# Kernel optimization log

Hardware: AMD Instinct MI355X
Metric: run time of the kernel (lower is better)

## Reference

```python
import jax, jax.numpy as jnp
import numpy as np

# Dims: B=batch, N_IN=input capsules, D_IN=input capsule dim,
#       J=output capsules (nb_capsules), C=output capsule dim (capsule_size)
B, N_IN, D_IN, J, C = 32, 2048, 16, 64, 32
ITERS = 5
EPS = 1e-7  # K.epsilon()


def squash(v):
    # Keras code: vector += eps; norm = sum(v^2, -1, keepdims); v * norm/(1+norm)/sqrt(norm)
    v = v + EPS
    n = jnp.sum(v * v, axis=-1, keepdims=True)
    return v * (n / (1.0 + n) / jnp.sqrt(n))


def setup_inputs() -> dict:
    key = jax.random.key(0)
    k1, k2 = jax.random.split(key)
    x = jax.random.normal(k1, (B, N_IN, D_IN, 1), dtype=jnp.float32)
    # glorot_uniform over fan_in=D_IN (last axis), fan_out=C
    limit = float(np.sqrt(6.0 / (D_IN + C)))
    W = jax.random.uniform(k2, (N_IN, J, C, D_IN), dtype=jnp.float32,
                           minval=-limit, maxval=limit)
    return {"x": x, "W": W}


def reference(x, W):
    # x: (B, N_IN, D_IN, 1) -> u: (B, N_IN, D_IN)
    u = x[..., 0]
    # Prediction vectors u_hat[b,i,j] = W[i,j] @ u[b,i] : (B, N_IN, J, C)
    u_hat = jnp.einsum('bid,ijcd->bijc', u, W)
    # Routing logits b_ij: (B, N_IN, J)
    b = jnp.zeros(u_hat.shape[:3], dtype=u_hat.dtype)
    v = None
    for i in range(ITERS):
        c = jax.nn.softmax(b, axis=1)              # softmax over input capsules (axis=1 in source)
        s = jnp.einsum('bij,bijc->bjc', c, u_hat)   # weighted sum over i -> (B, J, C)
        v = squash(s)                                # squash over capsule vector dim C
        if i < ITERS - 1:
            # agreement update: b += <v_j, u_hat_ij>
            b = b + jnp.einsum('bjc,bijc->bij', v, u_hat)
    # match compute_output_shape (B, nb_capsules, capsule_size, 1)
    return v[..., None]
```

## Files before the change

### kernel.cpp

```cpp
#include <hip/hip_runtime.h>
#include <hip/hip_bf16.h>

#define B_ 32
#define N_ 2048
#define D_ 16
#define J_ 64
#define C_ 32
#define NCHUNK 32
#define ICHUNK 64
#define IPW    16

typedef __attribute__((ext_vector_type(8)))  short short8;
typedef __attribute__((ext_vector_type(4)))  short s16x4;
typedef __attribute__((ext_vector_type(16))) float f32x16;
typedef __attribute__((ext_vector_type(4)))  float f32x4;
typedef __attribute__((ext_vector_type(16))) int   i32x16;
typedef __attribute__((ext_vector_type(2)))  long  longx2;

using bf16_t = __hip_bfloat16;

__global__ __launch_bounds__(256) void prep_u_kernel(const float* __restrict__ x,
                                                     bf16_t* __restrict__ ut,
                                                     signed char* __restrict__ uq,
                                                     float* __restrict__ su) {
  int t = blockIdx.x * 256 + threadIdx.x;
  int b = t & 31;
  int i = t >> 5;
  const float* xp = x + (size_t)(b * N_ + i) * D_;
  float v[16];
  *(f32x4*)(v)      = *(const f32x4*)(xp);
  *(f32x4*)(v + 4)  = *(const f32x4*)(xp + 4);
  *(f32x4*)(v + 8)  = *(const f32x4*)(xp + 8);
  *(f32x4*)(v + 12) = *(const f32x4*)(xp + 12);

  float m = 0.f;
#pragma unroll
  for (int k = 0; k < 16; ++k) m = fmaxf(m, fabsf(v[k]));
  m = fmaxf(m, 1e-20f);
  float inv = 127.0f / m;
  union { longx2 l2; signed char c[16]; } pk;
#pragma unroll
  for (int k = 0; k < 16; ++k) pk.c[k] = (signed char)__float2int_rn(v[k] * inv);
  *(longx2*)(uq + (size_t)t * D_) = pk.l2;
  su[t] = m * (1.0f / 127.0f);

  union { short8 s; bf16_t h[8]; } o0, o1;
#pragma unroll
  for (int k = 0; k < 8; ++k) { o0.h[k] = __float2bfloat16(v[k]); o1.h[k] = __float2bfloat16(v[8 + k]); }
  *(short8*)(ut + (size_t)t * D_)     = o0.s;
  *(short8*)(ut + (size_t)t * D_ + 8) = o1.s;
}

template<int MODE>
__global__ __launch_bounds__(256) void pass_kernel(
    const float*        __restrict__ Wf,
    const signed char*  __restrict__ Wq,
    signed char*        __restrict__ Wqo,
    float*              __restrict__ SWo,
    const float*        __restrict__ SW,
    const signed char*  __restrict__ uq,
    const float*        __restrict__ su,
    const bf16_t*       __restrict__ ut,
    const float*        __restrict__ V,
    float*              __restrict__ PS,
    float*              __restrict__ PZ)
{
  constexpr bool UNIFORM = (MODE == 0 || MODE == 2);
  constexpr bool INT8    = (MODE == 0 || MODE == 1);

  const int tid  = threadIdx.x;
  const int w    = tid >> 6;
  const int lane = tid & 63;
  const int half = lane >> 5;
  const int lc   = lane & 31;

  const int j  = blockIdx.x / NCHUNK;
  const int ch = blockIdx.x % NCHUNK;

  int crow[16];
#pragma unroll
  for (int r = 0; r < 16; ++r) crow[r] = (r & 3) + 4 * half + 8 * (r >> 2);

  float Vreg[16];
  if (!UNIFORM) {
#pragma unroll
    for (int r = 0; r < 16; ++r) Vreg[r] = V[(lc * J_ + j) * C_ + crow[r]];
  }

  float S[16];
#pragma unroll
  for (int r = 0; r < 16; ++r) S[r] = 0.f;
  float zacc = 0.f;

  const int ibase = ch * ICHUNK + w * IPW;
  const int frag_off = lc * D_ + half * 8;

  if constexpr (INT8) {
    const i32x16 zi = {0,0,0,0,0,0,0,0,0,0,0,0,0,0,0,0};
    for (int t = 0; t < IPW; ++t) {
      const int i = ibase + t;
      long ul = *(const long*)(uq + (size_t)i * (B_ * D_) + frag_off);
      const size_t tile = ((size_t)i * J_ + j) * (C_ * D_);
      long wl;
      float sw_i;
      if constexpr (MODE == 0) {
        const float* wp = Wf + tile + frag_off;
        f32x4 w0 = *(const f32x4*)(wp);
        f32x4 w1 = *(const f32x4*)(wp + 4);
        float wv[8] = {w0.x, w0.y, w0.z, w0.w, w1.x, w1.y, w1.z, w1.w};
        float m = 0.f;
#pragma unroll
        for (int k = 0; k < 8; ++k) m = fmaxf(m, fabsf(wv[k]));
        m = fmaxf(m, __shfl_xor(m, 1));
        m = fmaxf(m, __shfl_xor(m, 2));
        m = fmaxf(m, __shfl_xor(m, 4));
        m = fmaxf(m, __shfl_xor(m, 8));
        m = fmaxf(m, __shfl_xor(m, 16));
        m = fmaxf(m, __shfl_xor(m, 32));
        m = fmaxf(m, 1e-20f);
        float qs = 127.0f / m;
        union { long l; signed char c[8]; } pk;
#pragma unroll
        for (int k = 0; k < 8; ++k) pk.c[k] = (signed char)__float2int_rn(wv[k] * qs);
        wl = pk.l;
        sw_i = m * (1.0f / 127.0f);
        *(long*)(Wqo + tile + frag_off) = wl;
        if (lane == 0) SWo[(size_t)i * J_ + j] = sw_i;
      } else {
        wl = *(const long*)(Wq + tile + frag_off);
        sw_i = SW[(size_t)i * J_ + j];
      }
      const float s = sw_i * su[i * B_ + lc];

      i32x16 iacc = __builtin_amdgcn_mfma_i32_32x32x16_i8(wl, ul, zi, 0, 0, 0);

      if constexpr (UNIFORM) {
#pragma unroll
        for (int r = 0; r < 16; ++r) S[r] = fmaf(s, (float)iacc[r], S[r]);
      } else {
        float af[16];
        float ph = 0.f;
#pragma unroll
        for (int r = 0; r < 16; ++r) { af[r] = (float)iacc[r]; ph = fmaf(Vreg[r], af[r], ph); }
        ph *= s;
        ph += __shfl_xor(ph, 32);
        float e = __expf(ph);
        zacc += e;
        float es = e * s;
#pragma unroll
        for (int r = 0; r < 16; ++r) S[r] = fmaf(es, af[r], S[r]);
      }
    }
  } else {
    const f32x16 zeroacc = {0,0,0,0,0,0,0,0,0,0,0,0,0,0,0,0};
    for (int t = 0; t < IPW; ++t) {
      const int i = ibase + t;
      short8 ufrag = *(const short8*)(ut + (size_t)i * (B_ * D_) + frag_off);
      const size_t tile = ((size_t)i * J_ + j) * (C_ * D_);
      const float* wp = Wf + tile + frag_off;
      f32x4 w0 = *(const f32x4*)(wp);
      f32x4 w1 = *(const f32x4*)(wp + 4);
      union { short8 v; bf16_t h[8]; } cv;
      cv.h[0] = __float2bfloat16(w0.x);
      cv.h[1] = __float2bfloat16(w0.y);
      cv.h[2] = __float2bfloat16(w0.z);
      cv.h[3] = __float2bfloat16(w0.w);
      cv.h[4] = __float2bfloat16(w1.x);
      cv.h[5] = __float2bfloat16(w1.y);
      cv.h[6] = __float2bfloat16(w1.z);
      cv.h[7] = __float2bfloat16(w1.w);
      short8 wfrag = cv.v;

      f32x16 acc = __builtin_amdgcn_mfma_f32_32x32x16_bf16(wfrag, ufrag, zeroacc, 0, 0, 0);

      if constexpr (UNIFORM) {
#pragma unroll
        for (int r = 0; r < 16; ++r) S[r] += acc[r];
      } else {
        float ph = 0.f;
#pragma unroll
        for (int r = 0; r < 16; ++r) ph = fmaf(Vreg[r], acc[r], ph);
        ph += __shfl_xor(ph, 32);
        float e = __expf(ph);
        zacc += e;
#pragma unroll
        for (int r = 0; r < 16; ++r) S[r] = fmaf(e, acc[r], S[r]);
      }
    }
  }

  __shared__ float S_lds[4 * 32 * 33];
  __shared__ float Z_lds[4 * 32];
#pragma unroll
  for (int r = 0; r < 16; ++r)
    S_lds[w * 1056 + lc * 33 + crow[r]] = S[r];
  if (!half)
    Z_lds[w * 32 + lc] = UNIFORM ? (float)IPW : zacc;
  __syncthreads();

  const size_t pbase = (size_t)blockIdx.x * 1024;
  for (int e = tid; e < 1024; e += 256) {
    int b = e >> 5, c = e & 31;
    PS[pbase + e] = S_lds[b * 33 + c] + S_lds[1056 + b * 33 + c] +
                    S_lds[2112 + b * 33 + c] + S_lds[3168 + b * 33 + c];
  }
  if (tid < 32)
    PZ[(size_t)blockIdx.x * 32 + tid] =
        Z_lds[tid] + Z_lds[32 + tid] + Z_lds[64 + tid] + Z_lds[96 + tid];
}

__global__ __launch_bounds__(256) void combine_kernel(
    const float* __restrict__ PS, const float* __restrict__ PZ,
    float* __restrict__ V, float* __restrict__ out, int first, int last)
{
  int t  = blockIdx.x * 256 + threadIdx.x;
  int c  = t & 31;
  int bj = t >> 5;
  int b  = bj >> 6;
  int j  = bj & 63;
  float s = 0.f, zz = 0.f;
#pragma unroll
  for (int ch = 0; ch < NCHUNK; ++ch) {
    s  += PS[(size_t)(j * NCHUNK + ch) * 1024 + b * 32 + c];
    zz += PZ[(j * NCHUNK + ch) * 32 + b];
  }
  float sv = s / zz + 1e-7f;
  float n = sv * sv;
  n += __shfl_xor(n, 1);
  n += __shfl_xor(n, 2);
  n += __shfl_xor(n, 4);
  n += __shfl_xor(n, 8);
  n += __shfl_xor(n, 16);
  float f = n / ((1.f + n) * sqrtf(n));
  float v = sv * f;
  float Vn = first ? v : (V[t] + v);
  V[t] = Vn;
  if (last) out[t] = v;
}

extern "C" void kernel_launch(void* const* d_in, const int* in_sizes, int n_in,
                              void* d_out, int out_size, void* d_ws, size_t ws_size,
                              hipStream_t stream)
{
  const float* x  = (const float*)d_in[0];
  const float* Wf = (const float*)d_in[1];
  float* out = (float*)d_out;
  char* ws = (char*)d_ws;

  const size_t SZ_WQ = (size_t)N_ * J_ * C_ * D_;
  const size_t SZ_SW = (size_t)N_ * J_ * 4;
  const size_t SZ_UQ = (size_t)N_ * B_ * D_;
  const size_t SZ_SU = (size_t)N_ * B_ * 4;
  const size_t SZ_UT = (size_t)N_ * B_ * D_ * 2;
  const size_t SZ_V  = (size_t)B_ * J_ * C_ * 4;
  const size_t SZ_PS = (size_t)J_ * NCHUNK * B_ * C_ * 4;
  const size_t SZ_PZ = (size_t)J_ * NCHUNK * B_ * 4;

  const bool big = ws_size >= SZ_WQ + SZ_SW + SZ_UQ + SZ_SU + SZ_UT + SZ_V + SZ_PS + SZ_PZ;
  char* p = ws;
  signed char* Wq = nullptr;
  float* SWp = nullptr;
  if (big) {
    Wq  = (signed char*)p; p += SZ_WQ;
    SWp = (float*)p;       p += SZ_SW;
  }
  signed char* uq = (signed char*)p; p += SZ_UQ;
  float* su = (float*)p;             p += SZ_SU;
  bf16_t* ut = (bf16_t*)p;           p += SZ_UT;
  float*  V  = (float*)p;            p += SZ_V;
  float*  PS = (float*)p;            p += SZ_PS;
  float*  PZ = (float*)p;

  prep_u_kernel<<<dim3((N_ * B_) / 256), dim3(256), 0, stream>>>(x, ut, uq, su);

  dim3 gA(J_ * NCHUNK), blk(256), gB((B_ * J_ * C_) / 256);
  if (big) {
    pass_kernel<0><<<gA, blk, 0, stream>>>(Wf, nullptr, Wq, SWp, nullptr, uq, su, ut, nullptr, PS, PZ);
    combine_kernel<<<gB, blk, 0, stream>>>(PS, PZ, V, out, 1, 0);
    for (int it = 1; it < 5; ++it) {
      pass_kernel<1><<<gA, blk, 0, stream>>>(nullptr, Wq, nullptr, nullptr, SWp, uq, su, ut, V, PS, PZ);
      combine_kernel<<<gB, blk, 0, stream>>>(PS, PZ, V, out, 0, it == 4 ? 1 : 0);
    }
  } else {
    pass_kernel<2><<<gA, blk, 0, stream>>>(Wf, nullptr, nullptr, nullptr, nullptr, uq, su, ut, nullptr, PS, PZ);
    combine_kernel<<<gB, blk, 0, stream>>>(PS, PZ, V, out, 1, 0);
    for (int it = 1; it < 5; ++it) {
      pass_kernel<3><<<gA, blk, 0, stream>>>(Wf, nullptr, nullptr, nullptr, nullptr, uq, su, ut, V, PS, PZ);
      combine_kernel<<<gB, blk, 0, stream>>>(PS, PZ, V, out, 0, it == 4 ? 1 : 0);
    }
  }
}
```

Baseline: 513.9 us.

## Split W quantization into a separate kernel and prefetch int8 operands in pass loop

Moves the per-call fp32-to-int8 quantization of W out of the first routing pass into a dedicated grid-stride prep kernel, so that pass reads int8 weights like the later passes. The int8 pass loop now software-pipelines its loads, fetching the next weight fragment, u fragment and scale while the current MFMA and accumulation run. The prep kernel adds a launch and makes the first pass re-read the int8 weights it just wrote, in exchange for a simpler, better-overlapped inner loop in all five passes.

```diff
diff --git a/kernel.cpp b/kernel.cpp
--- a/kernel.cpp
+++ b/kernel.cpp
@@ -51,12 +51,40 @@
   *(short8*)(ut + (size_t)t * D_ + 8) = o1.s;
 }
 
+__global__ __launch_bounds__(256) void prep_w_kernel(const float* __restrict__ Wf,
+                                                     signed char* __restrict__ Wq,
+                                                     float* __restrict__ SW) {
+  const int lane = threadIdx.x & 63;
+  const int wid  = (blockIdx.x * 256 + threadIdx.x) >> 6;
+  const int nw   = gridDim.x * 4;
+  for (int tile = wid; tile < N_ * J_; tile += nw) {
+    const float* wp = Wf + (size_t)tile * (C_ * D_) + lane * 8;
+    f32x4 a = *(const f32x4*)wp;
+    f32x4 b = *(const f32x4*)(wp + 4);
+    float wv[8] = {a.x, a.y, a.z, a.w, b.x, b.y, b.z, b.w};
+    float m = 0.f;
+#pragma unroll
+    for (int k = 0; k < 8; ++k) m = fmaxf(m, fabsf(wv[k]));
+    m = fmaxf(m, __shfl_xor(m, 1));
+    m = fmaxf(m, __shfl_xor(m, 2));
+    m = fmaxf(m, __shfl_xor(m, 4));
+    m = fmaxf(m, __shfl_xor(m, 8));
+    m = fmaxf(m, __shfl_xor(m, 16));
+    m = fmaxf(m, __shfl_xor(m, 32));
+    m = fmaxf(m, 1e-20f);
+    float qs = 127.0f / m;
+    union { long l; signed char c[8]; } pk;
+#pragma unroll
+    for (int k = 0; k < 8; ++k) pk.c[k] = (signed char)__float2int_rn(wv[k] * qs);
+    *(long*)(Wq + (size_t)tile * (C_ * D_) + lane * 8) = pk.l;
+    if (lane == 0) SW[tile] = m * (1.0f / 127.0f);
+  }
+}
+
 template<int MODE>
 __global__ __launch_bounds__(256) void pass_kernel(
     const float*        __restrict__ Wf,
     const signed char*  __restrict__ Wq,
-    signed char*        __restrict__ Wqo,
-    float*              __restrict__ SWo,
     const float*        __restrict__ SW,
     const signed char*  __restrict__ uq,
     const float*        __restrict__ su,
@@ -97,59 +125,36 @@
 
   if constexpr (INT8) {
     const i32x16 zi = {0,0,0,0,0,0,0,0,0,0,0,0,0,0,0,0};
+    long wl = *(const long*)(Wq + ((size_t)ibase * J_ + j) * (C_ * D_) + frag_off);
+    long ul = *(const long*)(uq + (size_t)ibase * (B_ * D_) + frag_off);
+    float sc = SW[(size_t)ibase * J_ + j] * su[ibase * B_ + lc];
+
     for (int t = 0; t < IPW; ++t) {
-      const int i = ibase + t;
-      long ul = *(const long*)(uq + (size_t)i * (B_ * D_) + frag_off);
-      const size_t tile = ((size_t)i * J_ + j) * (C_ * D_);
-      long wl;
-      float sw_i;
-      if constexpr (MODE == 0) {
-        const float* wp = Wf + tile + frag_off;
-        f32x4 w0 = *(const f32x4*)(wp);
-        f32x4 w1 = *(const f32x4*)(wp + 4);
-        float wv[8] = {w0.x, w0.y, w0.z, w0.w, w1.x, w1.y, w1.z, w1.w};
-        float m = 0.f;
-#pragma unroll
-        for (int k = 0; k < 8; ++k) m = fmaxf(m, fabsf(wv[k]));
-        m = fmaxf(m, __shfl_xor(m, 1));
-        m = fmaxf(m, __shfl_xor(m, 2));
-        m = fmaxf(m, __shfl_xor(m, 4));
-        m = fmaxf(m, __shfl_xor(m, 8));
-        m = fmaxf(m, __shfl_xor(m, 16));
-        m = fmaxf(m, __shfl_xor(m, 32));
-        m = fmaxf(m, 1e-20f);
-        float qs = 127.0f / m;
-        union { long l; signed char c[8]; } pk;
-#pragma unroll
-        for (int k = 0; k < 8; ++k) pk.c[k] = (signed char)__float2int_rn(wv[k] * qs);
-        wl = pk.l;
-        sw_i = m * (1.0f / 127.0f);
-        *(long*)(Wqo + tile + frag_off) = wl;
-        if (lane == 0) SWo[(size_t)i * J_ + j] = sw_i;
-      } else {
-        wl = *(const long*)(Wq + tile + frag_off);
-        sw_i = SW[(size_t)i * J_ + j];
-      }
-      const float s = sw_i * su[i * B_ + lc];
+      const int tn = (t + 1 < IPW) ? t + 1 : t;
+      const int in_ = ibase + tn;
+      long wl_n = *(const long*)(Wq + ((size_t)in_ * J_ + j) * (C_ * D_) + frag_off);
+      long ul_n = *(const long*)(uq + (size_t)in_ * (B_ * D_) + frag_off);
+      float sc_n = SW[(size_t)in_ * J_ + j] * su[in_ * B_ + lc];
 
       i32x16 iacc = __builtin_amdgcn_mfma_i32_32x32x16_i8(wl, ul, zi, 0, 0, 0);
 
       if constexpr (UNIFORM) {
 #pragma unroll
-        for (int r = 0; r < 16; ++r) S[r] = fmaf(s, (float)iacc[r], S[r]);
+        for (int r = 0; r < 16; ++r) S[r] = fmaf(sc, (float)iacc[r], S[r]);
       } else {
         float af[16];
         float ph = 0.f;
 #pragma unroll
         for (int r = 0; r < 16; ++r) { af[r] = (float)iacc[r]; ph = fmaf(Vreg[r], af[r], ph); }
-        ph *= s;
+        ph *= sc;
         ph += __shfl_xor(ph, 32);
         float e = __expf(ph);
         zacc += e;
-        float es = e * s;
+        float es = e * sc;
 #pragma unroll
         for (int r = 0; r < 16; ++r) S[r] = fmaf(es, af[r], S[r]);
       }
+      wl = wl_n; ul = ul_n; sc = sc_n;
     }
   } else {
     const f32x16 zeroacc = {0,0,0,0,0,0,0,0,0,0,0,0,0,0,0,0};
@@ -275,17 +280,18 @@
 
   dim3 gA(J_ * NCHUNK), blk(256), gB((B_ * J_ * C_) / 256);
   if (big) {
-    pass_kernel<0><<<gA, blk, 0, stream>>>(Wf, nullptr, Wq, SWp, nullptr, uq, su, ut, nullptr, PS, PZ);
+    prep_w_kernel<<<dim3(2048), blk, 0, stream>>>(Wf, Wq, SWp);
+    pass_kernel<0><<<gA, blk, 0, stream>>>(nullptr, Wq, SWp, uq, su, nullptr, nullptr, PS, PZ);
     combine_kernel<<<gB, blk, 0, stream>>>(PS, PZ, V, out, 1, 0);
     for (int it = 1; it < 5; ++it) {
-      pass_kernel<1><<<gA, blk, 0, stream>>>(nullptr, Wq, nullptr, nullptr, SWp, uq, su, ut, V, PS, PZ);
+      pass_kernel<1><<<gA, blk, 0, stream>>>(nullptr, Wq, SWp, uq, su, nullptr, V, PS, PZ);
       combine_kernel<<<gB, blk, 0, stream>>>(PS, PZ, V, out, 0, it == 4 ? 1 : 0);
     }
   } else {
-    pass_kernel<2><<<gA, blk, 0, stream>>>(Wf, nullptr, nullptr, nullptr, nullptr, uq, su, ut, nullptr, PS, PZ);
+    pass_kernel<2><<<gA, blk, 0, stream>>>(Wf, nullptr, nullptr, uq, su, ut, nullptr, PS, PZ);
     combine_kernel<<<gB, blk, 0, stream>>>(PS, PZ, V, out, 1, 0);
     for (int it = 1; it < 5; ++it) {
-      pass_kernel<3><<<gA, blk, 0, stream>>>(Wf, nullptr, nullptr, nullptr, nullptr, uq, su, ut, V, PS, PZ);
+      pass_kernel<3><<<gA, blk, 0, stream>>>(Wf, nullptr, nullptr, uq, su, ut, V, PS, PZ);
       combine_kernel<<<gB, blk, 0, stream>>>(PS, PZ, V, out, 0, it == 4 ? 1 : 0);
     }
   }
```

Measured after the change: 512.2 us. Within noise of the previous version (-0.3%).
